# Optimization experiments

Hardware: AMD Instinct MI355X
Metric: run time of the kernel (lower is better)

Reference implementation:

```python
import jax, jax.numpy as jnp
import numpy as np

B = 32
SEQ_LEN = 512      # T and n_fft
PRED_LEN = 96      # STFT window_size = PRED_LEN // 2 = 48
TOP_K = 3
D_MODEL = 512
D_FF = 512
N_HEADS = 8
C_OUT = 32         # graph node count
NODE_DIM = 10
CONV_CH = 32
SKIP_CH = 32
GCN_DEPTH = 2
PROP_ALPHA = 0.05
HOP = 48
EPS = 1e-5


def layer_norm(x, g, b):
    m = x.mean(-1, keepdims=True)
    v = ((x - m) ** 2).mean(-1, keepdims=True)
    return (x - m) * jax.lax.rsqrt(v + EPS) * g + b


def stft_mag(x):
    """torch.stft(center=True, hann window of len 48 center-padded to n_fft) magnitude,
    vmapped over channels. Returns [B, frames, n_fft//2+1, N]."""
    n_fft = SEQ_LEN
    win_len = PRED_LEN // 2
    n = jnp.arange(win_len, dtype=x.dtype)
    win = 0.5 - 0.5 * jnp.cos(2.0 * jnp.pi * n / win_len)   # periodic hann
    pad_l = (n_fft - win_len) // 2
    win = jnp.pad(win, (pad_l, n_fft - win_len - pad_l))     # center-pad window to n_fft
    T = x.shape[1]
    xp = jnp.pad(x, ((0, 0), (n_fft // 2, n_fft // 2), (0, 0)), mode='reflect')
    nfr = T // HOP + 1
    idx = jnp.arange(nfr)[:, None] * HOP + jnp.arange(n_fft)[None, :]
    frames = xp[:, idx, :]                                   # [B, nfr, n_fft, N]
    spec = jnp.fft.rfft(frames * win[None, None, :, None], axis=2)
    return jnp.abs(spec)


def attention_block(x, wq, bq, wk, bk, wv, bv, wo, bo, ff1_w, ff1_b, ff2_w, ff2_b,
                    n1_g, n1_b, n2_g, n2_b):
    M, S, D = x.shape
    H, Dh = N_HEADS, D // N_HEADS
    q = (x @ wq.T + bq).reshape(M, S, H, Dh)
    k = (x @ wk.T + bk).reshape(M, S, H, Dh)
    v = (x @ wv.T + bv).reshape(M, S, H, Dh)
    scores = jnp.einsum('mshd,mthd->mhst', q, k) * (1.0 / float(np.sqrt(Dh)))
    o = jnp.einsum('mhst,mthd->mshd', jax.nn.softmax(scores, axis=-1), v).reshape(M, S, D)
    x1 = layer_norm(x + (o @ wo.T + bo), n1_g, n1_b)
    y = jax.nn.gelu(x1 @ ff1_w.T + ff1_b, approximate=False) @ ff2_w.T + ff2_b
    return layer_norm(x1 + y, n2_g, n2_b)


def graph_block(x, nv1, nv2, sw, sb, mw, mb, ew, eb, lw, lb, g, b):
    # adaptive adjacency over C_OUT nodes
    adp = jax.nn.softmax(jax.nn.relu(nv1 @ nv2), axis=1)
    adj = adp + jnp.eye(C_OUT, dtype=x.dtype)
    a = adj / adj.sum(1, keepdims=True)
    # start_conv: [B,1,D,T] -> [B,CONV_CH,C_OUT,T]
    h = jax.lax.conv_general_dilated(x.transpose(0, 2, 1)[:, None], sw, (1, 1), 'VALID',
                                     dimension_numbers=('NCHW', 'OIHW', 'NCHW'))
    h = h + sb[None, :, None, None]
    x0, outs = h, [h]
    for _ in range(GCN_DEPTH):  # mixprop
        h = PROP_ALPHA * x0 + (1.0 - PROP_ALPHA) * jnp.einsum('bcwt,vw->bcvt', h, a)
        outs.append(h)
    ho = jnp.einsum('oc,bcnt->bont', mw, jnp.concatenate(outs, axis=1)) + mb[None, :, None, None]
    h = jax.nn.gelu(ho, approximate=False)
    out = jnp.einsum('bcns,tcs->btn', h, ew) + eb[None, :, None]   # end_conv (1,seq_len) kernel
    out = out @ lw + lb                                            # Linear c_out -> d_model
    return layer_norm(x + out, g, b)


def setup_inputs() -> dict:
    ks = jax.random.split(jax.random.key(0), 32)
    r = lambda i, shape, s=0.02: jax.random.normal(ks[i], shape, jnp.float32) * s
    kh = D_MODEL - C_OUT + 1
    return {
        'x': jax.random.normal(ks[0], (B, SEQ_LEN, D_MODEL), jnp.float32),
        'nv1': r(1, (TOP_K, C_OUT, NODE_DIM), 1.0),
        'nv2': r(2, (TOP_K, NODE_DIM, C_OUT), 1.0),
        'start_w': r(3, (TOP_K, CONV_CH, 1, kh, 1)),
        'start_b': r(4, (TOP_K, CONV_CH)),
        'mix_w': r(5, (TOP_K, SKIP_CH, (GCN_DEPTH + 1) * CONV_CH)),
        'mix_b': r(6, (TOP_K, SKIP_CH)),
        'end_w': r(7, (TOP_K, SEQ_LEN, SKIP_CH, SEQ_LEN)),
        'end_b': r(8, (TOP_K, SEQ_LEN)),
        'glin_w': r(9, (TOP_K, C_OUT, D_MODEL)),
        'glin_b': r(10, (TOP_K, D_MODEL)),
        'gnorm_g': 1.0 + r(11, (TOP_K, D_MODEL), 0.1),
        'gnorm_b': r(12, (TOP_K, D_MODEL), 0.1),
        'wq': r(13, (D_MODEL, D_MODEL)), 'bq': r(14, (D_MODEL,)),
        'wk': r(15, (D_MODEL, D_MODEL)), 'bk': r(16, (D_MODEL,)),
        'wv': r(17, (D_MODEL, D_MODEL)), 'bv': r(18, (D_MODEL,)),
        'wo': r(19, (D_MODEL, D_MODEL)), 'bo': r(20, (D_MODEL,)),
        'ff1_w': r(21, (D_FF, D_MODEL)), 'ff1_b': r(22, (D_FF,)),
        'ff2_w': r(23, (D_MODEL, D_FF)), 'ff2_b': r(24, (D_MODEL,)),
        'an1_g': 1.0 + r(25, (D_MODEL,), 0.1), 'an1_b': r(26, (D_MODEL,), 0.1),
        'an2_g': 1.0 + r(27, (D_MODEL,), 0.1), 'an2_b': r(28, (D_MODEL,), 0.1),
        'norm_g': 1.0 + r(29, (D_MODEL,), 0.1), 'norm_b': r(30, (D_MODEL,), 0.1),
    }


def reference(x, nv1, nv2, start_w, start_b, mix_w, mix_b, end_w, end_b, glin_w, glin_b,
              gnorm_g, gnorm_b, wq, bq, wk, bk, wv, bv, wo, bo,
              ff1_w, ff1_b, ff2_w, ff2_b, an1_g, an1_b, an2_g, an2_b, norm_g, norm_b):
    Bx, T, N = x.shape
    mag = stft_mag(x)                                   # [B, frames, Fbins, N]
    freq = mag.mean(axis=(0, 1, 3)).at[0].set(0.0)
    top = np.asarray(jax.lax.top_k(freq, TOP_K)[1])     # concrete: shapes below are data-dependent
    periods = [int(T // int(f)) for f in top]
    sw = jax.nn.softmax(mag[:, :, top, :].mean(axis=(1, 3)), axis=1)  # [B, k] scale weights
    cur = x
    res = []
    for i in range(TOP_K):
        scale = periods[i]
        # NOTE: faithful to the original bug: x is overwritten by gconv output each iteration
        cur = graph_block(cur, nv1[i], nv2[i], start_w[i], start_b[i], mix_w[i], mix_b[i],
                          end_w[i], end_b[i], glin_w[i], glin_b[i], gnorm_g[i], gnorm_b[i])
        length = -(-T // scale) * scale
        out = jnp.pad(cur, ((0, 0), (0, length - T), (0, 0))) if length > T else cur
        out = out.reshape(Bx * (length // scale), scale, N)
        out = attention_block(out, wq, bq, wk, bk, wv, bv, wo, bo,
                              ff1_w, ff1_b, ff2_w, ff2_b, an1_g, an1_b, an2_g, an2_b)
        out = jax.nn.gelu(layer_norm(out, norm_g, norm_b), approximate=False)
        out = out.reshape(Bx, length, N)[:, :T]
        res.append(out)
    res = jnp.stack(res, axis=-1)                       # [B, T, N, k]
    return (res * sw[:, None, None, :]).sum(-1) + cur
```

## Files before the change

### kernel.cpp

```cpp
#include <hip/hip_runtime.h>
#include <math.h>

#define DI __device__ __forceinline__

namespace {
constexpr int B_ = 32;
constexpr int T_ = 512;
constexpr int N_ = 512;
constexpr int C_ = 32;
constexpr int KH_ = 481;
constexpr int HOP_ = 48;
constexpr int WIN_ = 48;
constexpr int NFR_ = 11;
constexpr int NBIN_ = 257;
constexpr int NSB_ = 8 * NFR_ * B_;
constexpr int TOKMAX = 21760;
constexpr int PLW = TOKMAX * 512;
constexpr float EPS_ = 1e-5f;

constexpr size_t MBY = 1ull << 20;
constexpr size_t OFF_META = 0;
constexpr size_t OFF_FREQ = 4096;
constexpr size_t OFF_SW   = 8192;
constexpr size_t OFF_BEFF = 16384;
constexpr size_t OFF_P12  = 32768;
constexpr size_t OFF_FSB  = 65536;
constexpr size_t OFF_OSM  = 1 * MBY;
constexpr size_t OFF_WB   = 4 * MBY;
constexpr size_t OFF_WDH  = 10 * MBY;
constexpr size_t OFF_EWH  = 12 * MBY;
constexpr size_t OFF_CUR  = 44 * MBY;
constexpr size_t OFF_ACC  = 76 * MBY;
constexpr size_t TR       = 108 * MBY;
constexpr size_t OFF_T    = TR;
constexpr size_t OFF_WPH  = TR + 6 * MBY;
constexpr size_t OFF_G    = TR + 64 * MBY;
constexpr size_t OFF_G2   = TR + 128 * MBY;
constexpr size_t OFF_PART = TR + 192 * MBY;
constexpr size_t OFF_A0 = TR;
constexpr size_t OFF_A2 = TR + 44 * MBY;
constexpr size_t OFF_A3 = TR + 88 * MBY;
constexpr size_t OFF_A4 = TR + 132 * MBY;
constexpr size_t OFF_A5 = TR + 176 * MBY;
constexpr size_t OFF_FP = TR;
}

typedef __attribute__((ext_vector_type(2))) float f32x2;
typedef __attribute__((ext_vector_type(4))) float f32x4;
typedef __attribute__((ext_vector_type(8))) short bf8;
typedef __attribute__((ext_vector_type(8))) unsigned short u16x8;

DI float gelu_exact(float x) { return 0.5f * x * (1.0f + erff(x * 0.7071067811865475f)); }
DI unsigned short f2bf(float f) {
  unsigned u = __float_as_uint(f);
  u += 0x7FFFu + ((u >> 16) & 1u);
  return (unsigned short)(u >> 16);
}
DI float bf2f(unsigned short s) { return __uint_as_float(((unsigned)s) << 16); }
DI float ld2(const unsigned short* __restrict__ H, const unsigned short* __restrict__ L,
             size_t i) { return bf2f(H[i]) + bf2f(L[i]); }
DI void st2(unsigned short* __restrict__ H, unsigned short* __restrict__ L,
            size_t i, float v) {
  unsigned short h = f2bf(v);
  H[i] = h;
  L[i] = f2bf(v - bf2f(h));
}
DI void gll16(const unsigned short* g, unsigned short* l) {
  __builtin_amdgcn_global_load_lds(
      (const __attribute__((address_space(1))) void*)g,
      (__attribute__((address_space(3))) void*)l, 16, 0, 0);
}

__global__ __launch_bounds__(256) void k_stft2(const float* __restrict__ x,
                                               float* __restrict__ fpart) {
  int bid = blockIdx.x;
  int cc = bid & 7;
  int f = (bid >> 3) % NFR_;
  int b = bid / (8 * NFR_);
  __shared__ float xw[WIN_][64];
  int tid = threadIdx.x;
  for (int i = tid; i < WIN_ * 64; i += 256) {
    int j = i >> 6, n = i & 63;
    int gi = f * HOP_ + 232 + j - 256;
    if (gi < 0) gi = -gi;
    float w = 0.5f - 0.5f * cosf((float)j * 0.13089969389957472f);
    xw[j][n] = w * x[((size_t)b * T_ + gi) * N_ + cc * 64 + n];
  }
  __syncthreads();
  for (int pair = tid; pair < NBIN_ * 8; pair += 256) {
    int k = pair >> 3;
    int c4 = (pair & 7) * 4;
    int r0 = (k * 232) & 511;
    float a0 = (float)r0 * 0.012271846303085130f;
    float c = cosf(a0), s = sinf(a0);
    float dA = (float)k * 0.012271846303085130f;
    float cd = cosf(dA), sd = sinf(dA);
    f32x2 ri[8];
#pragma unroll
    for (int q = 0; q < 8; ++q) ri[q] = (f32x2){0.f, 0.f};
#pragma unroll 4
    for (int j = 0; j < WIN_; ++j) {
      float4 v0 = *(const float4*)&xw[j][c4];
      float4 v1 = *(const float4*)&xw[j][32 + c4];
      f32x2 cs = (f32x2){c, s};
      ri[0] += v0.x * cs;
      ri[1] += v0.y * cs;
      ri[2] += v0.z * cs;
      ri[3] += v0.w * cs;
      ri[4] += v1.x * cs;
      ri[5] += v1.y * cs;
      ri[6] += v1.z * cs;
      ri[7] += v1.w * cs;
      float cn = c * cd - s * sd;
      s = s * cd + c * sd;
      c = cn;
    }
    float m = 0.f;
#pragma unroll
    for (int q = 0; q < 8; ++q) m += sqrtf(ri[q].x * ri[q].x + ri[q].y * ri[q].y);
    for (int off = 4; off > 0; off >>= 1) m += __shfl_xor(m, off);
    if ((tid & 7) == 0) fpart[(size_t)k * NSB_ + bid] = m;
  }
}

__global__ __launch_bounds__(256) void k_fred(const float* __restrict__ fpart,
                                              float* __restrict__ freq,
                                              float* __restrict__ fsumb) {
  int k = blockIdx.x;
  int tid = threadIdx.x;
  int b = tid >> 3, j = tid & 7;
  float s = 0.f;
  for (int i = j; i < 88; i += 8) s += fpart[(size_t)k * NSB_ + b * 88 + i];
  for (int off = 4; off > 0; off >>= 1) s += __shfl_xor(s, off);
  __shared__ float bs[32];
  if (j == 0) bs[b] = s;
  __syncthreads();
  if (tid < 32) {
    float v = bs[tid];
    fsumb[k * 32 + tid] = v;
    for (int off = 16; off > 0; off >>= 1) v += __shfl_xor(v, off);
    if (tid == 0) freq[k] = v;
  }
}

__global__ void k_topk(const float* __restrict__ freq, int* __restrict__ meta) {
  if (threadIdx.x == 0 && blockIdx.x == 0) {
    float bv[3] = {-1e30f, -1e30f, -1e30f};
    int bi[3] = {1, 1, 1};
    for (int k = 1; k < NBIN_; ++k) {
      float v = freq[k];
      if (v > bv[0]) { bv[2]=bv[1]; bi[2]=bi[1]; bv[1]=bv[0]; bi[1]=bi[0]; bv[0]=v; bi[0]=k; }
      else if (v > bv[1]) { bv[2]=bv[1]; bi[2]=bi[1]; bv[1]=v; bi[1]=k; }
      else if (v > bv[2]) { bv[2]=v; bi[2]=k; }
    }
    for (int i = 0; i < 3; ++i) {
      int top = bi[i];
      int p = T_ / top;
      int L = ((T_ + p - 1) / p) * p;
      meta[i] = top;
      meta[3 + i] = p;
      meta[6 + i] = L;
      meta[9 + i] = L / p;
      meta[15 + i] = B_ * L;
    }
  }
}

__global__ void k_sw2(const float* __restrict__ fsumb, const int* __restrict__ meta,
                      float* __restrict__ swb) {
  int b = threadIdx.x;
  if (b < B_) {
    float inv = 1.0f / (float)(NFR_ * N_);
    float m0 = fsumb[meta[0] * 32 + b] * inv;
    float m1 = fsumb[meta[1] * 32 + b] * inv;
    float m2 = fsumb[meta[2] * 32 + b] * inv;
    float mx = fmaxf(m0, fmaxf(m1, m2));
    float e0 = expf(m0 - mx), e1 = expf(m1 - mx), e2 = expf(m2 - mx);
    float s = e0 + e1 + e2;
    swb[b * 4 + 0] = e0 / s; swb[b * 4 + 1] = e1 / s; swb[b * 4 + 2] = e2 / s;
  }
}

__global__ __launch_bounds__(1024) void k_adjprep(const float* __restrict__ nv1,
                                                  const float* __restrict__ nv2,
                                                  const float* __restrict__ mw,
                                                  const float* __restrict__ mb,
                                                  const float* __restrict__ sb,
                                                  float* __restrict__ P12,
                                                  float* __restrict__ beff) {
  __shared__ float A32s[32][32];
  __shared__ float Ms[32][32], P1s[32][32], P2s[32][32], S1[32], S2[32], sbl[32];
  int tid = threadIdx.x;
  if (tid < 32) {
    int v = tid;
    float row[32];
    for (int w = 0; w < 32; ++w) {
      float s = 0.f;
      for (int d = 0; d < 10; ++d) s += nv1[v * 10 + d] * nv2[d * 32 + w];
      row[w] = fmaxf(s, 0.f);
    }
    float mx = -1e30f;
    for (int w = 0; w < 32; ++w) mx = fmaxf(mx, row[w]);
    float sm = 0.f;
    for (int w = 0; w < 32; ++w) { row[w] = expf(row[w] - mx); sm += row[w]; }
    for (int w = 0; w < 32; ++w) row[w] /= sm;
    row[v] += 1.0f;
    float rs = 0.f;
    for (int w = 0; w < 32; ++w) rs += row[w];
    for (int w = 0; w < 32; ++w) A32s[v][w] = row[w] / rs;
    sbl[tid] = sb[tid];
  }
  __syncthreads();
  int w = tid >> 5, v = tid & 31;
  Ms[w][v] = A32s[v][w];
  __syncthreads();
  float p1 = 0.95f * Ms[w][v] + (w == v ? 0.05f : 0.f);
  P1s[w][v] = p1;
  __syncthreads();
  float p2 = 0.f;
  for (int u = 0; u < 32; ++u) p2 += P1s[w][u] * Ms[u][v];
  p2 = 0.95f * p2 + (w == v ? 0.05f : 0.f);
  P2s[w][v] = p2;
  P12[tid] = p1;
  P12[1024 + tid] = p2;
  __syncthreads();
  if (tid < 32) {
    float s1 = 0.f, s2 = 0.f;
    for (int u = 0; u < 32; ++u) { s1 += P1s[u][tid]; s2 += P2s[u][tid]; }
    S1[tid] = s1; S2[tid] = s2;
  }
  __syncthreads();
  int o = w;
  float be = mb[o];
  for (int c = 0; c < 32; ++c) {
    float sc = sbl[c];
    be += mw[o * 96 + c] * sc;
    be += mw[o * 96 + 32 + c] * sc * S1[v];
    be += mw[o * 96 + 64 + c] * sc * S2[v];
  }
  beff[tid] = be;
}

__global__ __launch_bounds__(256) void k_T(const float* __restrict__ P12,
                                           const float* __restrict__ mw,
                                           float* __restrict__ Tm) {
  int idx = blockIdx.x * 256 + threadIdx.x;
  int r = idx >> 10, k2 = idx & 1023;
  int o = r >> 5, v = r & 31;
  int c = k2 >> 5, w = k2 & 31;
  float t = mw[o * 96 + 32 + c] * P12[w * 32 + v]
          + mw[o * 96 + 64 + c] * P12[1024 + w * 32 + v];
  if (w == v) t += mw[o * 96 + c];
  Tm[idx] = t;
}

__global__ void k_wdh(const float* __restrict__ swi, unsigned short* __restrict__ WH) {
  int idx = blockIdx.x * 256 + threadIdx.x;
  int j = idx >> 10, k2 = idx & 1023;
  int c = k2 >> 5, w = k2 & 31;
  int kk = j - w;
  float vv = (kk >= 0 && kk < KH_) ? swi[c * KH_ + kk] : 0.f;
  WH[idx] = f2bf(vv);
}

__global__ void k_splith(const float* __restrict__ src, unsigned short* __restrict__ Hi,
                         int n) {
  int i = blockIdx.x * 256 + threadIdx.x;
  if (i * 4 >= n) return;
  float4 v = *(const float4*)&src[i * 4];
  ushort4 h;
  h.x = f2bf(v.x); h.y = f2bf(v.y); h.z = f2bf(v.z); h.w = f2bf(v.w);
  *(ushort4*)&Hi[i * 4] = h;
}

__global__ __launch_bounds__(256, 2) void k_mm2(
    const float* __restrict__ A, const unsigned short* __restrict__ Bh,
    const float* __restrict__ bias,
    float* __restrict__ C, float* __restrict__ Cpart,
    int M, int N, int K, int lda, int dogelu) {
  const int bm = blockIdx.y * 128;
  if (bm >= M) return;
  const int bn = blockIdx.x * 128;
  const int nz = gridDim.z, z = blockIdx.z;
  const int kpb = K / nz;
  const int kbeg = z * kpb, kend = kbeg + kpb;

  __shared__ __align__(16) unsigned short AhS[4096], AlS[4096], BhS[4096];

  const int tid = threadIdx.x;
  const int wave = tid >> 6, lane = tid & 63;
  const int wr = wave >> 1, wc = wave & 1;
  const int fr = lane & 15, fs = lane >> 4;

  const int sr = tid >> 1, ss = (tid & 1) * 2;
  const int sx = (sr >> 1) & 3;
  const int so0 = sr * 32 + 8 * (ss ^ sx);
  const int so1 = sr * 32 + 8 * ((ss + 1) ^ sx);

  const int row0 = tid >> 2;
  const int s0 = (tid & 3) ^ ((row0 >> 1) & 3);
  const unsigned short* gBh0 = Bh + (size_t)(bn + row0) * K + s0 * 8;
  const unsigned short* gBh1 = gBh0 + (size_t)64 * K;
  unsigned short* lB0 = &BhS[wave * 512];
  unsigned short* lB1 = &BhS[2048 + wave * 512];

  int aoff[4], boff[4];
#pragma unroll
  for (int m = 0; m < 4; ++m) {
    int ra = wr * 64 + m * 16 + fr;
    aoff[m] = ra * 32 + 8 * (fs ^ ((ra >> 1) & 3));
    int rb = wc * 64 + m * 16 + fr;
    boff[m] = rb * 32 + 8 * (fs ^ ((rb >> 1) & 3));
  }

  const bool aok = (bm + sr) < M;
  const float* Arow = A + (size_t)(bm + sr) * lda + ss * 8;

  f32x4 acc[4][4];
#pragma unroll
  for (int m = 0; m < 4; ++m)
#pragma unroll
    for (int n = 0; n < 4; ++n) acc[m][n] = (f32x4){0.f, 0.f, 0.f, 0.f};

  for (int k0 = kbeg; k0 < kend; k0 += 32) {
    float4 a0, a1, a2, a3;
    if (aok) {
      const float4* p = (const float4*)(Arow + k0);
      a0 = p[0]; a1 = p[1]; a2 = p[2]; a3 = p[3];
    } else {
      a0 = a1 = a2 = a3 = make_float4(0.f, 0.f, 0.f, 0.f);
    }
    float av[16];
    av[0]=a0.x; av[1]=a0.y; av[2]=a0.z; av[3]=a0.w;
    av[4]=a1.x; av[5]=a1.y; av[6]=a1.z; av[7]=a1.w;
    av[8]=a2.x; av[9]=a2.y; av[10]=a2.z; av[11]=a2.w;
    av[12]=a3.x; av[13]=a3.y; av[14]=a3.z; av[15]=a3.w;
    u16x8 h0, h1, l0, l1;
#pragma unroll
    for (int j = 0; j < 8; ++j) {
      unsigned u = __float_as_uint(av[j]);
      h0[j] = (unsigned short)(u >> 16);
      float r2 = av[j] - __uint_as_float(u & 0xffff0000u);
      l0[j] = (unsigned short)(__float_as_uint(r2) >> 16);
      unsigned u2 = __float_as_uint(av[j + 8]);
      h1[j] = (unsigned short)(u2 >> 16);
      float r3 = av[j + 8] - __uint_as_float(u2 & 0xffff0000u);
      l1[j] = (unsigned short)(__float_as_uint(r3) >> 16);
    }
    __syncthreads();
    gll16(gBh0 + k0, lB0); gll16(gBh1 + k0, lB1);
    *(u16x8*)&AhS[so0] = h0; *(u16x8*)&AhS[so1] = h1;
    *(u16x8*)&AlS[so0] = l0; *(u16x8*)&AlS[so1] = l1;
    __syncthreads();
    bf8 ah[4], al4[4], bh4[4];
#pragma unroll
    for (int m = 0; m < 4; ++m) {
      ah[m]  = *(const bf8*)&AhS[aoff[m]];
      al4[m] = *(const bf8*)&AlS[aoff[m]];
    }
#pragma unroll
    for (int n = 0; n < 4; ++n) bh4[n] = *(const bf8*)&BhS[boff[n]];
#pragma unroll
    for (int m = 0; m < 4; ++m)
#pragma unroll
      for (int n = 0; n < 4; ++n) {
        acc[m][n] = __builtin_amdgcn_mfma_f32_16x16x32_bf16(ah[m],  bh4[n], acc[m][n], 0, 0, 0);
        acc[m][n] = __builtin_amdgcn_mfma_f32_16x16x32_bf16(al4[m], bh4[n], acc[m][n], 0, 0, 0);
      }
  }

  if (nz > 1) {
    float* P = Cpart + (size_t)z * M * N;
#pragma unroll
    for (int m = 0; m < 4; ++m)
#pragma unroll
      for (int r = 0; r < 4; ++r) {
        int row = bm + wr * 64 + m * 16 + fs * 4 + r;
        if (row < M) {
#pragma unroll
          for (int n = 0; n < 4; ++n) {
            int col = bn + wc * 64 + n * 16 + fr;
            P[(size_t)row * N + col] = acc[m][n][r];
          }
        }
      }
  } else {
    float bcol[4];
#pragma unroll
    for (int n = 0; n < 4; ++n) bcol[n] = bias ? bias[bn + wc * 64 + n * 16 + fr] : 0.f;
#pragma unroll
    for (int m = 0; m < 4; ++m)
#pragma unroll
      for (int r = 0; r < 4; ++r) {
        int row = bm + wr * 64 + m * 16 + fs * 4 + r;
        if (row < M) {
#pragma unroll
          for (int n = 0; n < 4; ++n) {
            int col = bn + wc * 64 + n * 16 + fr;
            float v = acc[m][n][r] + bcol[n];
            if (dogelu) v = gelu_exact(v);
            C[(size_t)row * N + col] = v;
          }
        }
      }
  }
}

__global__ __launch_bounds__(256, 4) void k_mmb1(
    const unsigned short* __restrict__ Ah,
    const unsigned short* __restrict__ Bh,
    const float* __restrict__ bias,
    unsigned short* __restrict__ Ch, unsigned short* __restrict__ Cl,
    int M, int N, int K, const int* __restrict__ Mdyn, int dogelu) {
  if (Mdyn) M = *Mdyn;
  const int bm = blockIdx.y * 128;
  if (bm >= M) return;
  const int bn = blockIdx.x * 128;

  __shared__ __align__(16) unsigned short AhS[4096], BhS[4096];

  const int tid = threadIdx.x;
  const int wave = tid >> 6, lane = tid & 63;
  const int wr = wave >> 1, wc = wave & 1;
  const int fr = lane & 15, fs = lane >> 4;

  const int row0 = tid >> 2;
  const int s0 = (tid & 3) ^ ((row0 >> 1) & 3);
  const unsigned short* gAh0 = Ah + (size_t)(bm + row0) * K + s0 * 8;
  const unsigned short* gAh1 = gAh0 + (size_t)64 * K;
  const unsigned short* gBh0 = Bh + (size_t)(bn + row0) * K + s0 * 8;
  const unsigned short* gBh1 = gBh0 + (size_t)64 * K;
  const int lb0 = wave * 512, lb1 = 2048 + wave * 512;

  int aoff[4], boff[4];
#pragma unroll
  for (int m = 0; m < 4; ++m) {
    int ra = wr * 64 + m * 16 + fr;
    aoff[m] = ra * 32 + 8 * (fs ^ ((ra >> 1) & 3));
    int rb = wc * 64 + m * 16 + fr;
    boff[m] = rb * 32 + 8 * (fs ^ ((rb >> 1) & 3));
  }

  f32x4 acc[4][4];
#pragma unroll
  for (int m = 0; m < 4; ++m)
#pragma unroll
    for (int n = 0; n < 4; ++n) acc[m][n] = (f32x4){0.f, 0.f, 0.f, 0.f};

  for (int k0 = 0; k0 < K; k0 += 32) {
    __syncthreads();
    gll16(gAh0 + k0, &AhS[lb0]); gll16(gAh1 + k0, &AhS[lb1]);
    gll16(gBh0 + k0, &BhS[lb0]); gll16(gBh1 + k0, &BhS[lb1]);
    __syncthreads();
    bf8 ah[4], bh4[4];
#pragma unroll
    for (int m = 0; m < 4; ++m) ah[m] = *(const bf8*)&AhS[aoff[m]];
#pragma unroll
    for (int n = 0; n < 4; ++n) bh4[n] = *(const bf8*)&BhS[boff[n]];
#pragma unroll
    for (int m = 0; m < 4; ++m)
#pragma unroll
      for (int n = 0; n < 4; ++n)
        acc[m][n] = __builtin_amdgcn_mfma_f32_16x16x32_bf16(ah[m], bh4[n], acc[m][n], 0, 0, 0);
  }

  float bcol[4];
#pragma unroll
  for (int n = 0; n < 4; ++n) bcol[n] = bias[bn + wc * 64 + n * 16 + fr];
#pragma unroll
  for (int m = 0; m < 4; ++m)
#pragma unroll
    for (int r = 0; r < 4; ++r) {
      int row = bm + wr * 64 + m * 16 + fs * 4 + r;
      if (row < M) {
#pragma unroll
        for (int n = 0; n < 4; ++n) {
          int col = bn + wc * 64 + n * 16 + fr;
          float v = acc[m][n][r] + bcol[n];
          if (dogelu) v = gelu_exact(v);
          size_t o = (size_t)row * N + col;
          unsigned short h = f2bf(v);
          Ch[o] = h;
          Cl[o] = f2bf(v - bf2f(h));
        }
      }
    }
}

__global__ void k_red16(const float* __restrict__ part, const float* __restrict__ eb,
                        float* __restrict__ dst) {
  int idx = blockIdx.x * 256 + threadIdx.x;
  float s = eb ? eb[idx & 511] : 0.f;
#pragma unroll
  for (int zz = 0; zz < 16; ++zz) s += part[(size_t)zz * 524288 + idx];
  dst[idx] = s;
}

__global__ void k_redsplit(const float* __restrict__ part, unsigned short* __restrict__ WH) {
  int idx = blockIdx.x * 256 + threadIdx.x;
  float s = 0.f;
#pragma unroll
  for (int zz = 0; zz < 8; ++zz) s += part[(size_t)zz * 524288 + idx];
  WH[idx] = f2bf(s);
}

__global__ __launch_bounds__(256) void k_repack(const float* __restrict__ G,
                                                float* __restrict__ G2) {
  int bid = blockIdx.x;
  int st = bid & 15, c = (bid >> 4) & 31, b = bid >> 9;
  __shared__ float tile[32][33];
  int tid = threadIdx.x;
  int n = tid & 31, s = tid >> 5;
  for (int q = 0; q < 4; ++q) {
    int ss = s + q * 8;
    tile[ss][n] = G[((size_t)b * T_ + st * 32 + ss) * 1024 + c * 32 + n];
  }
  __syncthreads();
  int s2 = tid & 31, n2 = tid >> 5;
  for (int q = 0; q < 4; ++q) {
    int nn = n2 + q * 8;
    G2[((size_t)b * 32 + nn) * 16384 + c * 512 + st * 32 + s2] = tile[s2][nn];
  }
}

__global__ __launch_bounds__(256) void k_lwln(const float* __restrict__ osm,
                                              const float* __restrict__ lw,
                                              const float* __restrict__ lb,
                                              const float* __restrict__ curIn,
                                              const float* __restrict__ g,
                                              const float* __restrict__ bt,
                                              float* __restrict__ curOut,
                                              unsigned short* __restrict__ xh,
                                              unsigned short* __restrict__ xl,
                                              const int* __restrict__ meta, int iter) {
  int tok = blockIdx.x;
  int b = tok >> 9, t = tok & 511;
  __shared__ float os[C_];
  __shared__ float red[256];
  int tid = threadIdx.x;
  if (tid < C_) os[tid] = osm[((size_t)b * C_ + tid) * T_ + t];
  __syncthreads();
  float val[2];
#pragma unroll
  for (int q = 0; q < 2; ++q) {
    int m = tid + q * 256;
    float s = lb[m] + curIn[(size_t)tok * N_ + m];
    for (int n2 = 0; n2 < C_; ++n2) s += os[n2] * lw[n2 * N_ + m];
    val[q] = s;
  }
  red[tid] = val[0] + val[1];
  __syncthreads();
  for (int off = 128; off > 0; off >>= 1) { if (tid < off) red[tid] += red[tid + off]; __syncthreads(); }
  float mean = red[0] * (1.0f / N_);
  __syncthreads();
  float d0 = val[0] - mean, d1 = val[1] - mean;
  red[tid] = d0 * d0 + d1 * d1;
  __syncthreads();
  for (int off = 128; off > 0; off >>= 1) { if (tid < off) red[tid] += red[tid + off]; __syncthreads(); }
  float inv = rsqrtf(red[0] * (1.0f / N_) + EPS_);
  float o0 = d0 * inv * g[tid] + bt[tid];
  float o1 = d1 * inv * g[tid + 256] + bt[tid + 256];
  curOut[(size_t)tok * N_ + tid] = o0;
  curOut[(size_t)tok * N_ + tid + 256] = o1;
  int L = meta[6 + iter];
  size_t pi = ((size_t)b * L + t) * N_;
  st2(xh, xl, pi + tid, o0);
  st2(xh, xl, pi + tid + 256, o1);
}

__global__ void k_padtail(unsigned short* __restrict__ xh, unsigned short* __restrict__ xl,
                          const int* __restrict__ meta, int iter) {
  int L = meta[6 + iter];
  int pad = L - T_;
  if (pad <= 0) return;
  size_t total = (size_t)B_ * pad * N_;
  for (size_t idx = (size_t)blockIdx.x * 256 + threadIdx.x; idx < total;
       idx += (size_t)gridDim.x * 256) {
    size_t row = idx >> 9;
    int d = (int)(idx & 511);
    int b = (int)(row / pad), l = T_ + (int)(row % pad);
    size_t o = ((size_t)b * L + l) * N_ + d;
    xh[o] = 0; xl[o] = 0;
  }
}

__global__ __launch_bounds__(256) void k_lnadd(const unsigned short* __restrict__ r1h,
                                               const unsigned short* __restrict__ r1l,
                                               const unsigned short* __restrict__ r2h,
                                               const unsigned short* __restrict__ r2l,
                                               const float* __restrict__ g,
                                               const float* __restrict__ bt,
                                               unsigned short* __restrict__ dh,
                                               unsigned short* __restrict__ dl,
                                               const int* __restrict__ meta, int iter) {
  int tokens = meta[15 + iter];
  int tok = blockIdx.x;
  if (tok >= tokens) return;
  __shared__ float red[256];
  int tid = threadIdx.x;
  float val[2];
#pragma unroll
  for (int q = 0; q < 2; ++q) {
    size_t i = (size_t)tok * N_ + tid + q * 256;
    val[q] = ld2(r1h, r1l, i) + ld2(r2h, r2l, i);
  }
  red[tid] = val[0] + val[1];
  __syncthreads();
  for (int off = 128; off > 0; off >>= 1) { if (tid < off) red[tid] += red[tid + off]; __syncthreads(); }
  float mean = red[0] * (1.0f / N_);
  __syncthreads();
  float d0 = val[0] - mean, d1 = val[1] - mean;
  red[tid] = d0 * d0 + d1 * d1;
  __syncthreads();
  for (int off = 128; off > 0; off >>= 1) { if (tid < off) red[tid] += red[tid + off]; __syncthreads(); }
  float inv = rsqrtf(red[0] * (1.0f / N_) + EPS_);
  st2(dh, dl, (size_t)tok * N_ + tid, d0 * inv * g[tid] + bt[tid]);
  st2(dh, dl, (size_t)tok * N_ + tid + 256, d1 * inv * g[tid + 256] + bt[tid + 256]);
}

__global__ __launch_bounds__(256) void k_lnfin(const unsigned short* __restrict__ r1h,
                                               const unsigned short* __restrict__ r1l,
                                               const unsigned short* __restrict__ r2h,
                                               const unsigned short* __restrict__ r2l,
                                               const float* __restrict__ g1,
                                               const float* __restrict__ b1,
                                               const float* __restrict__ g2,
                                               const float* __restrict__ b2,
                                               const float* __restrict__ swb,
                                               float* __restrict__ acc,
                                               const int* __restrict__ meta, int iter) {
  int L = meta[6 + iter];
  int tok = blockIdx.x;
  if (tok >= B_ * L) return;
  int b = tok / L, l = tok % L;
  if (l >= T_) return;
  __shared__ float red[256];
  int tid = threadIdx.x;
  float val[2];
#pragma unroll
  for (int q = 0; q < 2; ++q) {
    size_t i = (size_t)tok * N_ + tid + q * 256;
    val[q] = ld2(r1h, r1l, i) + ld2(r2h, r2l, i);
  }
  red[tid] = val[0] + val[1];
  __syncthreads();
  for (int off = 128; off > 0; off >>= 1) { if (tid < off) red[tid] += red[tid + off]; __syncthreads(); }
  float mean = red[0] * (1.0f / N_);
  __syncthreads();
  float d0 = val[0] - mean, d1 = val[1] - mean;
  red[tid] = d0 * d0 + d1 * d1;
  __syncthreads();
  for (int off = 128; off > 0; off >>= 1) { if (tid < off) red[tid] += red[tid + off]; __syncthreads(); }
  float inv = rsqrtf(red[0] * (1.0f / N_) + EPS_);
  float y0 = d0 * inv * g1[tid] + b1[tid];
  float y1 = d1 * inv * g1[tid + 256] + b1[tid + 256];
  __syncthreads();
  red[tid] = y0 + y1;
  __syncthreads();
  for (int off = 128; off > 0; off >>= 1) { if (tid < off) red[tid] += red[tid + off]; __syncthreads(); }
  float mean2 = red[0] * (1.0f / N_);
  __syncthreads();
  float e0 = y0 - mean2, e1 = y1 - mean2;
  red[tid] = e0 * e0 + e1 * e1;
  __syncthreads();
  for (int off = 128; off > 0; off >>= 1) { if (tid < off) red[tid] += red[tid + off]; __syncthreads(); }
  float inv2 = rsqrtf(red[0] * (1.0f / N_) + EPS_);
  float s = swb[b * 4 + iter];
  float u0 = gelu_exact(e0 * inv2 * g2[tid] + b2[tid]);
  float u1 = gelu_exact(e1 * inv2 * g2[tid + 256] + b2[tid + 256]);
  size_t o = ((size_t)b * T_ + l) * N_;
  acc[o + tid] += s * u0;
  acc[o + tid + 256] += s * u1;
}

__global__ __launch_bounds__(256) void k_attn32(
    const unsigned short* __restrict__ qh, const unsigned short* __restrict__ ql,
    const unsigned short* __restrict__ kh, const unsigned short* __restrict__ kl,
    const unsigned short* __restrict__ vh, const unsigned short* __restrict__ vl,
    unsigned short* __restrict__ oh, unsigned short* __restrict__ ol,
    const int* __restrict__ meta, int iter) {
  (void)vl;
  int S = meta[3 + iter];
  if (S > 32) return;
  int L = meta[6 + iter], nseq = meta[9 + iter];
  int npair = B_ * nseq * 8;
  __shared__ float Kt[4][64 * 33];
  __shared__ unsigned short Vsh[4][32 * 66];
  __shared__ float qs[4][64];
  int tid = threadIdx.x;
  int wave = tid >> 6, lane = tid & 63;
  float* Ktw = Kt[wave];
  unsigned short* Vw = Vsh[wave];
  int gw = (blockIdx.x * 256 + tid) >> 6;
  int nw = (gridDim.x * 256) >> 6;
  const int tt = lane & 31;
  const int hf = lane >> 5;
  for (int pair = gw; pair < npair; pair += nw) {
    int h = pair & 7;
    int m = pair >> 3;
    int b = m / nseq, g2 = m - b * nseq;
    size_t base = ((size_t)b * L + (size_t)g2 * S) * N_ + h * 64;
    for (int i = lane; i < S * 64; i += 64) {
      int t = i >> 6, d = i & 63;
      size_t gi = base + (size_t)t * N_ + d;
      Ktw[d * 33 + t] = ld2(kh, kl, gi);
      Vw[t * 66 + d] = vh[gi];
    }
    bool tok = tt < S;
    for (int s = 0; s < S; ++s) {
      qs[wave][lane] = ld2(qh, ql, base + (size_t)s * N_ + lane);
      float part = 0.f;
      if (tok) {
        const float* kp = &Ktw[hf * 32 * 33 + tt];
        const float* qp = &qs[wave][hf * 32];
#pragma unroll 8
        for (int j = 0; j < 32; ++j) part += qp[j] * kp[j * 33];
      }
      part += __shfl_xor(part, 32);
      float sc = tok ? part * 0.125f : -3.0e38f;
      float mx = sc;
      for (int off = 16; off > 0; off >>= 1) mx = fmaxf(mx, __shfl_xor(mx, off));
      float p = tok ? expf(sc - mx) : 0.f;
      float ssum = p;
      for (int off = 16; off > 0; off >>= 1) ssum += __shfl_xor(ssum, off);
      float ov = 0.f;
      for (int t = 0; t < S; ++t) {
        float pt = __shfl(p, t);
        ov += pt * bf2f(Vw[t * 66 + lane]);
      }
      st2(oh, ol, base + (size_t)s * N_ + lane, ov / ssum);
    }
  }
}

__global__ __launch_bounds__(512) void k_attn_small(
    const unsigned short* __restrict__ qh, const unsigned short* __restrict__ ql,
    const unsigned short* __restrict__ kh, const unsigned short* __restrict__ kl,
    const unsigned short* __restrict__ vh, const unsigned short* __restrict__ vl,
    unsigned short* __restrict__ oh, unsigned short* __restrict__ ol,
    const int* __restrict__ meta, int iter) {
  int S = meta[3 + iter];
  if (S <= 32 || S > 128) return;
  int L = meta[6 + iter], nseq = meta[9 + iter];
  int M = B_ * nseq;
  int mh = blockIdx.x;
  int m = mh >> 3, h = mh & 7;
  if (m >= M) return;
  int b = m / nseq, g2 = m % nseq;
  size_t tok0 = (size_t)b * L + (size_t)g2 * S;
  __shared__ float Ks[64 * 129];
  __shared__ float Vs[128 * 65];
  __shared__ float qrow[8][64];
  __shared__ float Pr[8][128];
  int tid = threadIdx.x;
  for (int i = tid; i < S * 64; i += 512) {
    int t = i >> 6, d = i & 63;
    size_t gi = (tok0 + t) * N_ + h * 64 + d;
    float kv = ld2(kh, kl, gi);
    Ks[d * 129 + t] = kv;
    Vs[t * 65 + d] = ld2(vh, vl, gi);
  }
  __syncthreads();
  int wave = tid >> 6, lane = tid & 63;
  for (int s = wave; s < S; s += 8) {
    qrow[wave][lane] = ld2(qh, ql, (tok0 + s) * N_ + h * 64 + lane);
    float sc0 = -3.0e38f, sc1 = -3.0e38f;
    if (lane < S) {
      float ad = 0.f;
#pragma unroll 16
      for (int j = 0; j < 64; ++j) ad += qrow[wave][j] * Ks[j * 129 + lane];
      sc0 = ad * 0.125f;
    }
    if (S > 64 && lane + 64 < S) {
      float ad = 0.f;
#pragma unroll 16
      for (int j = 0; j < 64; ++j) ad += qrow[wave][j] * Ks[j * 129 + lane + 64];
      sc1 = ad * 0.125f;
    }
    float mx = fmaxf(sc0, sc1);
    for (int off = 32; off > 0; off >>= 1) mx = fmaxf(mx, __shfl_xor(mx, off));
    float e0 = (lane < S) ? expf(sc0 - mx) : 0.f;
    float e1 = (S > 64 && lane + 64 < S) ? expf(sc1 - mx) : 0.f;
    if (lane < S) Pr[wave][lane] = e0;
    if (S > 64 && lane + 64 < S) Pr[wave][lane + 64] = e1;
    float ssum = e0 + e1;
    for (int off = 32; off > 0; off >>= 1) ssum += __shfl_xor(ssum, off);
    float ov = 0.f;
#pragma unroll 8
    for (int t = 0; t < S; ++t) ov += Pr[wave][t] * Vs[t * 65 + lane];
    st2(oh, ol, (tok0 + s) * N_ + h * 64 + lane, ov / ssum);
  }
}

__global__ __launch_bounds__(256) void k_attn_big(
    const unsigned short* __restrict__ qh, const unsigned short* __restrict__ ql,
    const unsigned short* __restrict__ kh, const unsigned short* __restrict__ kl,
    const unsigned short* __restrict__ vh, const unsigned short* __restrict__ vl,
    unsigned short* __restrict__ oh, unsigned short* __restrict__ ol,
    const int* __restrict__ meta, int iter) {
  (void)kl; (void)vl;
  int p = meta[3 + iter];
  if (p <= 128) return;
  int L = meta[6 + iter], nseq = meta[9 + iter];
  int M = B_ * nseq;
  int mh = blockIdx.x;
  int m = mh >> 3, h = mh & 7;
  if (m >= M) return;
  int S = p;
  int b = m / nseq, g2 = m % nseq;
  size_t tok0 = (size_t)b * L + (size_t)g2 * S;
  __shared__ unsigned short Ks[512 * 66];
  __shared__ unsigned short Vs[512 * 66];
  __shared__ float qrow[4][64];
  __shared__ float Pr[4][512];
  int tid = threadIdx.x;
  for (int i = tid; i < S * 64; i += 256) {
    int t = i >> 6, d = i & 63;
    size_t gi = (tok0 + t) * N_ + h * 64 + d;
    Ks[t * 66 + d] = kh[gi];
    Vs[t * 66 + d] = vh[gi];
  }
  __syncthreads();
  int wave = tid >> 6, lane = tid & 63;
  for (int s = wave; s < S; s += 4) {
    qrow[wave][lane] = ld2(qh, ql, (tok0 + s) * N_ + h * 64 + lane);
    const float2* qp = (const float2*)&qrow[wave][0];
    float sc[8];
    float mx = -3.0e38f;
#pragma unroll
    for (int c2 = 0; c2 < 8; ++c2) {
      int t = lane + c2 * 64;
      float sv = -3.0e38f;
      if (t < S) {
        const unsigned int* kp = (const unsigned int*)&Ks[t * 66];
        float ad = 0.f;
#pragma unroll
        for (int j2 = 0; j2 < 32; ++j2) {
          float2 qq = qp[j2];
          unsigned int kw = kp[j2];
          ad += qq.x * bf2f((unsigned short)(kw & 0xffffu));
          ad += qq.y * bf2f((unsigned short)(kw >> 16));
        }
        sv = ad * 0.125f;
      }
      sc[c2] = sv;
      mx = fmaxf(mx, sv);
    }
    for (int off = 32; off > 0; off >>= 1) mx = fmaxf(mx, __shfl_xor(mx, off));
    float ssum = 0.f;
#pragma unroll
    for (int c2 = 0; c2 < 8; ++c2) {
      int t = lane + c2 * 64;
      float e = 0.f;
      if (t < S) { e = expf(sc[c2] - mx); Pr[wave][t] = e; }
      ssum += e;
    }
    for (int off = 32; off > 0; off >>= 1) ssum += __shfl_xor(ssum, off);
    float inv = 1.0f / ssum;
    float ov = 0.f;
#pragma unroll 8
    for (int t = 0; t < S; ++t) ov += Pr[wave][t] * bf2f(Vs[t * 66 + lane]);
    st2(oh, ol, (tok0 + s) * N_ + h * 64 + lane, ov * inv);
  }
}

__global__ void k_final(const float* __restrict__ acc, const float* __restrict__ cur,
                        float* __restrict__ out) {
  size_t idx = (size_t)blockIdx.x * 256 + threadIdx.x;
  out[idx] = acc[idx] + cur[idx];
}

extern "C" void kernel_launch(void* const* d_in, const int* in_sizes, int n_in,
                              void* d_out, int out_size, void* d_ws, size_t ws_size,
                              hipStream_t stream) {
  (void)in_sizes; (void)n_in; (void)out_size; (void)ws_size;
  const float* x       = (const float*)d_in[0];
  const float* nv1     = (const float*)d_in[1];
  const float* nv2     = (const float*)d_in[2];
  const float* start_w = (const float*)d_in[3];
  const float* start_b = (const float*)d_in[4];
  const float* mix_w   = (const float*)d_in[5];
  const float* mix_b   = (const float*)d_in[6];
  const float* end_w   = (const float*)d_in[7];
  const float* end_b   = (const float*)d_in[8];
  const float* glin_w  = (const float*)d_in[9];
  const float* glin_b  = (const float*)d_in[10];
  const float* gnorm_g = (const float*)d_in[11];
  const float* gnorm_b = (const float*)d_in[12];
  const float* wq = (const float*)d_in[13];
  const float* bq = (const float*)d_in[14];
  const float* wk = (const float*)d_in[15];
  const float* bk = (const float*)d_in[16];
  const float* wv = (const float*)d_in[17];
  const float* bv = (const float*)d_in[18];
  const float* wo = (const float*)d_in[19];
  const float* bo = (const float*)d_in[20];
  const float* ff1w = (const float*)d_in[21];
  const float* ff1b = (const float*)d_in[22];
  const float* ff2w = (const float*)d_in[23];
  const float* ff2b = (const float*)d_in[24];
  const float* an1g = (const float*)d_in[25];
  const float* an1b = (const float*)d_in[26];
  const float* an2g = (const float*)d_in[27];
  const float* an2b = (const float*)d_in[28];
  const float* nrmg = (const float*)d_in[29];
  const float* nrmb = (const float*)d_in[30];

  char* ws = (char*)d_ws;
  int*   meta = (int*)(ws + OFF_META);
  float* freq = (float*)(ws + OFF_FREQ);
  float* swb  = (float*)(ws + OFF_SW);
  float* beff = (float*)(ws + OFF_BEFF);
  float* P12  = (float*)(ws + OFF_P12);
  float* fsumb = (float*)(ws + OFF_FSB);
  float* osm  = (float*)(ws + OFF_OSM);
  unsigned short* WB  = (unsigned short*)(ws + OFF_WB);
  unsigned short* WdH = (unsigned short*)(ws + OFF_WDH);
  unsigned short* EWH = (unsigned short*)(ws + OFF_EWH);
  float* cur  = (float*)(ws + OFF_CUR);
  float* accb = (float*)(ws + OFF_ACC);
  float* fpart = (float*)(ws + OFF_FP);
  float* Tm   = (float*)(ws + OFF_T);
  unsigned short* WPH = (unsigned short*)(ws + OFF_WPH);
  float* G    = (float*)(ws + OFF_G);
  float* G2   = (float*)(ws + OFF_G2);
  float* PART = (float*)(ws + OFF_PART);
  unsigned short* A0h = (unsigned short*)(ws + OFF_A0); unsigned short* A0l = A0h + PLW;
  unsigned short* A2h = (unsigned short*)(ws + OFF_A2); unsigned short* A2l = A2h + PLW;
  unsigned short* A3h = (unsigned short*)(ws + OFF_A3); unsigned short* A3l = A3h + PLW;
  unsigned short* A4h = (unsigned short*)(ws + OFF_A4); unsigned short* A4l = A4h + PLW;
  unsigned short* A5h = (unsigned short*)(ws + OFF_A5); unsigned short* A5l = A5h + PLW;

  hipMemsetAsync(accb, 0, (size_t)B_ * T_ * N_ * 4, stream);

  k_stft2<<<NSB_, 256, 0, stream>>>(x, fpart);
  k_fred<<<NBIN_, 256, 0, stream>>>(fpart, freq, fsumb);
  k_topk<<<1, 64, 0, stream>>>(freq, meta);
  k_sw2<<<1, 64, 0, stream>>>(fsumb, meta, swb);

  const float* wlist[6] = {wq, wk, wv, wo, ff1w, ff2w};
  for (int w = 0; w < 6; ++w)
    k_splith<<<256, 256, 0, stream>>>(wlist[w], WB + (size_t)w * 262144, 262144);
  unsigned short* WqH = WB;
  unsigned short* WkH = WB + 262144;
  unsigned short* WvH = WB + 2 * 262144;
  unsigned short* WoH = WB + 3 * 262144;
  unsigned short* F1H = WB + 4 * 262144;
  unsigned short* F2H = WB + 5 * 262144;

  const float* curIn = x;
  for (int i = 0; i < 3; ++i) {
    k_adjprep<<<1, 1024, 0, stream>>>(nv1 + i * C_ * 10, nv2 + i * 10 * C_,
                                      mix_w + i * C_ * 96, mix_b + i * C_,
                                      start_b + i * C_, P12, beff);
    k_T<<<4096, 256, 0, stream>>>(P12, mix_w + i * C_ * 96, Tm);
    k_wdh<<<2048, 256, 0, stream>>>(start_w + i * C_ * KH_, WdH);
    k_mm2<<<dim3(4, 8, 8), 256, 0, stream>>>(Tm, WdH, nullptr, nullptr, PART,
                                             1024, 512, 1024, 1024, 0);
    k_redsplit<<<2048, 256, 0, stream>>>(PART, WPH);
    k_mm2<<<dim3(8, 128, 1), 256, 0, stream>>>(curIn, WPH, beff, G, nullptr,
                                               16384, 1024, 512, 512, 1);
    k_repack<<<B_ * C_ * 16, 256, 0, stream>>>(G, G2);
    k_splith<<<8192, 256, 0, stream>>>(end_w + (size_t)i * 8388608, EWH, 8388608);
    k_mm2<<<dim3(4, 8, 16), 256, 0, stream>>>(G2, EWH, nullptr, nullptr, PART,
                                              1024, 512, 16384, 16384, 0);
    k_red16<<<2048, 256, 0, stream>>>(PART, end_b + i * T_, osm);
    k_lwln<<<B_ * T_, 256, 0, stream>>>(osm, glin_w + i * C_ * N_, glin_b + i * N_, curIn,
                                        gnorm_g + i * N_, gnorm_b + i * N_, cur,
                                        A0h, A0l, meta, i);
    k_padtail<<<512, 256, 0, stream>>>(A0h, A0l, meta, i);
    const int* Mdyn = meta + 15 + i;
    dim3 gT(4, TOKMAX / 128, 1);
    k_mmb1<<<gT, 256, 0, stream>>>(A0h, WqH, bq, A2h, A2l, TOKMAX, 512, 512, Mdyn, 0);
    k_mmb1<<<gT, 256, 0, stream>>>(A0h, WkH, bk, A3h, A3l, TOKMAX, 512, 512, Mdyn, 0);
    k_mmb1<<<gT, 256, 0, stream>>>(A0h, WvH, bv, A4h, A4l, TOKMAX, 512, 512, Mdyn, 0);
    k_attn32<<<2048, 256, 0, stream>>>(A2h, A2l, A3h, A3l, A4h, A4l, A5h, A5l, meta, i);
    k_attn_small<<<4096, 512, 0, stream>>>(A2h, A2l, A3h, A3l, A4h, A4l, A5h, A5l, meta, i);
    k_attn_big<<<1024, 256, 0, stream>>>(A2h, A2l, A3h, A3l, A4h, A4l, A5h, A5l, meta, i);
    k_mmb1<<<gT, 256, 0, stream>>>(A5h, WoH, bo, A2h, A2l, TOKMAX, 512, 512, Mdyn, 0);
    k_lnadd<<<TOKMAX, 256, 0, stream>>>(A0h, A0l, A2h, A2l, an1g, an1b, A3h, A3l, meta, i);
    k_mmb1<<<gT, 256, 0, stream>>>(A3h, F1H, ff1b, A4h, A4l, TOKMAX, 512, 512, Mdyn, 1);
    k_mmb1<<<gT, 256, 0, stream>>>(A4h, F2H, ff2b, A5h, A5l, TOKMAX, 512, 512, Mdyn, 0);
    k_lnfin<<<TOKMAX, 256, 0, stream>>>(A3h, A3l, A5h, A5l, an2g, an2b, nrmg, nrmb,
                                        swb, accb, meta, i);
    curIn = cur;
  }
  k_final<<<(B_ * T_ * N_) / 256, 256, 0, stream>>>(accb, curIn, (float*)d_out);
}
```

Measured before the change: 2.207 ms.

## Fuse QKV projections into one GEMM and drop low-half bf16 split for attention

```diff
diff --git a/kernel.cpp b/kernel.cpp
--- a/kernel.cpp
+++ b/kernel.cpp
@@ -143,8 +143,11 @@
   }
 }
 
-__global__ void k_topk(const float* __restrict__ freq, int* __restrict__ meta) {
-  if (threadIdx.x == 0 && blockIdx.x == 0) {
+__global__ void k_topk(const float* __restrict__ freq, const float* __restrict__ fsumb,
+                       int* __restrict__ meta, float* __restrict__ swb) {
+  __shared__ int stop[3];
+  int tid = threadIdx.x;
+  if (tid == 0) {
     float bv[3] = {-1e30f, -1e30f, -1e30f};
     int bi[3] = {1, 1, 1};
     for (int k = 1; k < NBIN_; ++k) {
@@ -162,18 +165,16 @@
       meta[6 + i] = L;
       meta[9 + i] = L / p;
       meta[15 + i] = B_ * L;
-    }
-  }
-}
-
-__global__ void k_sw2(const float* __restrict__ fsumb, const int* __restrict__ meta,
-                      float* __restrict__ swb) {
-  int b = threadIdx.x;
+      stop[i] = top;
+    }
+  }
+  __syncthreads();
+  int b = tid;
   if (b < B_) {
     float inv = 1.0f / (float)(NFR_ * N_);
-    float m0 = fsumb[meta[0] * 32 + b] * inv;
-    float m1 = fsumb[meta[1] * 32 + b] * inv;
-    float m2 = fsumb[meta[2] * 32 + b] * inv;
+    float m0 = fsumb[stop[0] * 32 + b] * inv;
+    float m1 = fsumb[stop[1] * 32 + b] * inv;
+    float m2 = fsumb[stop[2] * 32 + b] * inv;
     float mx = fmaxf(m0, fmaxf(m1, m2));
     float e0 = expf(m0 - mx), e1 = expf(m1 - mx), e2 = expf(m2 - mx);
     float s = e0 + e1 + e2;
@@ -481,7 +482,89 @@
           size_t o = (size_t)row * N + col;
           unsigned short h = f2bf(v);
           Ch[o] = h;
-          Cl[o] = f2bf(v - bf2f(h));
+          if (Cl) Cl[o] = f2bf(v - bf2f(h));
+        }
+      }
+    }
+}
+
+__global__ __launch_bounds__(256, 4) void k_mmqkv(
+    const unsigned short* __restrict__ Ah,
+    const unsigned short* __restrict__ Bh,
+    const float* __restrict__ bq, const float* __restrict__ bk,
+    const float* __restrict__ bv,
+    unsigned short* __restrict__ Qh, unsigned short* __restrict__ Kh,
+    unsigned short* __restrict__ Vh,
+    int M, int K, const int* __restrict__ Mdyn) {
+  if (Mdyn) M = *Mdyn;
+  const int bm = blockIdx.y * 128;
+  if (bm >= M) return;
+  const int bn = blockIdx.x * 128;
+  const int sel = bn >> 9;
+  unsigned short* Ch = sel == 0 ? Qh : (sel == 1 ? Kh : Vh);
+  const float* bias = sel == 0 ? bq : (sel == 1 ? bk : bv);
+  const int cb = bn & 511;
+
+  __shared__ __align__(16) unsigned short AhS[4096], BhS[4096];
+
+  const int tid = threadIdx.x;
+  const int wave = tid >> 6, lane = tid & 63;
+  const int wr = wave >> 1, wc = wave & 1;
+  const int fr = lane & 15, fs = lane >> 4;
+
+  const int row0 = tid >> 2;
+  const int s0 = (tid & 3) ^ ((row0 >> 1) & 3);
+  const unsigned short* gAh0 = Ah + (size_t)(bm + row0) * K + s0 * 8;
+  const unsigned short* gAh1 = gAh0 + (size_t)64 * K;
+  const unsigned short* gBh0 = Bh + (size_t)(bn + row0) * K + s0 * 8;
+  const unsigned short* gBh1 = gBh0 + (size_t)64 * K;
+  const int lb0 = wave * 512, lb1 = 2048 + wave * 512;
+
+  int aoff[4], boff[4];
+#pragma unroll
+  for (int m = 0; m < 4; ++m) {
+    int ra = wr * 64 + m * 16 + fr;
+    aoff[m] = ra * 32 + 8 * (fs ^ ((ra >> 1) & 3));
+    int rb = wc * 64 + m * 16 + fr;
+    boff[m] = rb * 32 + 8 * (fs ^ ((rb >> 1) & 3));
+  }
+
+  f32x4 acc[4][4];
+#pragma unroll
+  for (int m = 0; m < 4; ++m)
+#pragma unroll
+    for (int n = 0; n < 4; ++n) acc[m][n] = (f32x4){0.f, 0.f, 0.f, 0.f};
+
+  for (int k0 = 0; k0 < K; k0 += 32) {
+    __syncthreads();
+    gll16(gAh0 + k0, &AhS[lb0]); gll16(gAh1 + k0, &AhS[lb1]);
+    gll16(gBh0 + k0, &BhS[lb0]); gll16(gBh1 + k0, &BhS[lb1]);
+    __syncthreads();
+    bf8 ah[4], bh4[4];
+#pragma unroll
+    for (int m = 0; m < 4; ++m) ah[m] = *(const bf8*)&AhS[aoff[m]];
+#pragma unroll
+    for (int n = 0; n < 4; ++n) bh4[n] = *(const bf8*)&BhS[boff[n]];
+#pragma unroll
+    for (int m = 0; m < 4; ++m)
+#pragma unroll
+      for (int n = 0; n < 4; ++n)
+        acc[m][n] = __builtin_amdgcn_mfma_f32_16x16x32_bf16(ah[m], bh4[n], acc[m][n], 0, 0, 0);
+  }
+
+  float bcol[4];
+#pragma unroll
+  for (int n = 0; n < 4; ++n) bcol[n] = bias[cb + wc * 64 + n * 16 + fr];
+#pragma unroll
+  for (int m = 0; m < 4; ++m)
+#pragma unroll
+    for (int r = 0; r < 4; ++r) {
+      int row = bm + wr * 64 + m * 16 + fs * 4 + r;
+      if (row < M) {
+#pragma unroll
+        for (int n = 0; n < 4; ++n) {
+          int col = cb + wc * 64 + n * 16 + fr;
+          Ch[(size_t)row * 512 + col] = f2bf(acc[m][n][r] + bcol[n]);
         }
       }
     }
@@ -674,12 +757,11 @@
 }
 
 __global__ __launch_bounds__(256) void k_attn32(
-    const unsigned short* __restrict__ qh, const unsigned short* __restrict__ ql,
-    const unsigned short* __restrict__ kh, const unsigned short* __restrict__ kl,
-    const unsigned short* __restrict__ vh, const unsigned short* __restrict__ vl,
-    unsigned short* __restrict__ oh, unsigned short* __restrict__ ol,
+    const unsigned short* __restrict__ qh,
+    const unsigned short* __restrict__ kh,
+    const unsigned short* __restrict__ vh,
+    unsigned short* __restrict__ oh,
     const int* __restrict__ meta, int iter) {
-  (void)vl;
   int S = meta[3 + iter];
   if (S > 32) return;
   int L = meta[6 + iter], nseq = meta[9 + iter];
@@ -703,12 +785,12 @@
     for (int i = lane; i < S * 64; i += 64) {
       int t = i >> 6, d = i & 63;
       size_t gi = base + (size_t)t * N_ + d;
-      Ktw[d * 33 + t] = ld2(kh, kl, gi);
+      Ktw[d * 33 + t] = bf2f(kh[gi]);
       Vw[t * 66 + d] = vh[gi];
     }
     bool tok = tt < S;
     for (int s = 0; s < S; ++s) {
-      qs[wave][lane] = ld2(qh, ql, base + (size_t)s * N_ + lane);
+      qs[wave][lane] = bf2f(qh[base + (size_t)s * N_ + lane]);
       float part = 0.f;
       if (tok) {
         const float* kp = &Ktw[hf * 32 * 33 + tt];
@@ -728,16 +810,16 @@
         float pt = __shfl(p, t);
         ov += pt * bf2f(Vw[t * 66 + lane]);
       }
-      st2(oh, ol, base + (size_t)s * N_ + lane, ov / ssum);
+      oh[base + (size_t)s * N_ + lane] = f2bf(ov / ssum);
     }
   }
 }
 
 __global__ __launch_bounds__(512) void k_attn_small(
-    const unsigned short* __restrict__ qh, const unsigned short* __restrict__ ql,
-    const unsigned short* __restrict__ kh, const unsigned short* __restrict__ kl,
-    const unsigned short* __restrict__ vh, const unsigned short* __restrict__ vl,
-    unsigned short* __restrict__ oh, unsigned short* __restrict__ ol,
+    const unsigned short* __restrict__ qh,
+    const unsigned short* __restrict__ kh,
+    const unsigned short* __restrict__ vh,
+    unsigned short* __restrict__ oh,
     const int* __restrict__ meta, int iter) {
   int S = meta[3 + iter];
   if (S <= 32 || S > 128) return;
@@ -756,14 +838,13 @@
   for (int i = tid; i < S * 64; i += 512) {
     int t = i >> 6, d = i & 63;
     size_t gi = (tok0 + t) * N_ + h * 64 + d;
-    float kv = ld2(kh, kl, gi);
-    Ks[d * 129 + t] = kv;
-    Vs[t * 65 + d] = ld2(vh, vl, gi);
+    Ks[d * 129 + t] = bf2f(kh[gi]);
+    Vs[t * 65 + d] = bf2f(vh[gi]);
   }
   __syncthreads();
   int wave = tid >> 6, lane = tid & 63;
   for (int s = wave; s < S; s += 8) {
-    qrow[wave][lane] = ld2(qh, ql, (tok0 + s) * N_ + h * 64 + lane);
+    qrow[wave][lane] = bf2f(qh[(tok0 + s) * N_ + h * 64 + lane]);
     float sc0 = -3.0e38f, sc1 = -3.0e38f;
     if (lane < S) {
       float ad = 0.f;
@@ -788,17 +869,16 @@
     float ov = 0.f;
 #pragma unroll 8
     for (int t = 0; t < S; ++t) ov += Pr[wave][t] * Vs[t * 65 + lane];
-    st2(oh, ol, (tok0 + s) * N_ + h * 64 + lane, ov / ssum);
+    oh[(tok0 + s) * N_ + h * 64 + lane] = f2bf(ov / ssum);
   }
 }
 
 __global__ __launch_bounds__(256) void k_attn_big(
-    const unsigned short* __restrict__ qh, const unsigned short* __restrict__ ql,
-    const unsigned short* __restrict__ kh, const unsigned short* __restrict__ kl,
-    const unsigned short* __restrict__ vh, const unsigned short* __restrict__ vl,
-    unsigned short* __restrict__ oh, unsigned short* __restrict__ ol,
+    const unsigned short* __restrict__ qh,
+    const unsigned short* __restrict__ kh,
+    const unsigned short* __restrict__ vh,
+    unsigned short* __restrict__ oh,
     const int* __restrict__ meta, int iter) {
-  (void)kl; (void)vl;
   int p = meta[3 + iter];
   if (p <= 128) return;
   int L = meta[6 + iter], nseq = meta[9 + iter];
@@ -823,7 +903,7 @@
   __syncthreads();
   int wave = tid >> 6, lane = tid & 63;
   for (int s = wave; s < S; s += 4) {
-    qrow[wave][lane] = ld2(qh, ql, (tok0 + s) * N_ + h * 64 + lane);
+    qrow[wave][lane] = bf2f(qh[(tok0 + s) * N_ + h * 64 + lane]);
     const float2* qp = (const float2*)&qrow[wave][0];
     float sc[8];
     float mx = -3.0e38f;
@@ -860,7 +940,7 @@
     float ov = 0.f;
 #pragma unroll 8
     for (int t = 0; t < S; ++t) ov += Pr[wave][t] * bf2f(Vs[t * 66 + lane]);
-    st2(oh, ol, (tok0 + s) * N_ + h * 64 + lane, ov * inv);
+    oh[(tok0 + s) * N_ + h * 64 + lane] = f2bf(ov * inv);
   }
 }
 
@@ -928,22 +1008,19 @@
   unsigned short* A0h = (unsigned short*)(ws + OFF_A0); unsigned short* A0l = A0h + PLW;
   unsigned short* A2h = (unsigned short*)(ws + OFF_A2); unsigned short* A2l = A2h + PLW;
   unsigned short* A3h = (unsigned short*)(ws + OFF_A3); unsigned short* A3l = A3h + PLW;
-  unsigned short* A4h = (unsigned short*)(ws + OFF_A4); unsigned short* A4l = A4h + PLW;
+  unsigned short* A4h = (unsigned short*)(ws + OFF_A4);
   unsigned short* A5h = (unsigned short*)(ws + OFF_A5); unsigned short* A5l = A5h + PLW;
 
   hipMemsetAsync(accb, 0, (size_t)B_ * T_ * N_ * 4, stream);
 
   k_stft2<<<NSB_, 256, 0, stream>>>(x, fpart);
   k_fred<<<NBIN_, 256, 0, stream>>>(fpart, freq, fsumb);
-  k_topk<<<1, 64, 0, stream>>>(freq, meta);
-  k_sw2<<<1, 64, 0, stream>>>(fsumb, meta, swb);
+  k_topk<<<1, 64, 0, stream>>>(freq, fsumb, meta, swb);
 
   const float* wlist[6] = {wq, wk, wv, wo, ff1w, ff2w};
   for (int w = 0; w < 6; ++w)
     k_splith<<<256, 256, 0, stream>>>(wlist[w], WB + (size_t)w * 262144, 262144);
-  unsigned short* WqH = WB;
-  unsigned short* WkH = WB + 262144;
-  unsigned short* WvH = WB + 2 * 262144;
+  unsigned short* WqkvH = WB;
   unsigned short* WoH = WB + 3 * 262144;
   unsigned short* F1H = WB + 4 * 262144;
   unsigned short* F2H = WB + 5 * 262144;
@@ -971,15 +1048,14 @@
     k_padtail<<<512, 256, 0, stream>>>(A0h, A0l, meta, i);
     const int* Mdyn = meta + 15 + i;
     dim3 gT(4, TOKMAX / 128, 1);
-    k_mmb1<<<gT, 256, 0, stream>>>(A0h, WqH, bq, A2h, A2l, TOKMAX, 512, 512, Mdyn, 0);
-    k_mmb1<<<gT, 256, 0, stream>>>(A0h, WkH, bk, A3h, A3l, TOKMAX, 512, 512, Mdyn, 0);
-    k_mmb1<<<gT, 256, 0, stream>>>(A0h, WvH, bv, A4h, A4l, TOKMAX, 512, 512, Mdyn, 0);
-    k_attn32<<<2048, 256, 0, stream>>>(A2h, A2l, A3h, A3l, A4h, A4l, A5h, A5l, meta, i);
-    k_attn_small<<<4096, 512, 0, stream>>>(A2h, A2l, A3h, A3l, A4h, A4l, A5h, A5l, meta, i);
-    k_attn_big<<<1024, 256, 0, stream>>>(A2h, A2l, A3h, A3l, A4h, A4l, A5h, A5l, meta, i);
+    k_mmqkv<<<dim3(12, TOKMAX / 128), 256, 0, stream>>>(A0h, WqkvH, bq, bk, bv,
+                                                        A2h, A3h, A4h, TOKMAX, 512, Mdyn);
+    k_attn32<<<2048, 256, 0, stream>>>(A2h, A3h, A4h, A5h, meta, i);
+    k_attn_small<<<4096, 512, 0, stream>>>(A2h, A3h, A4h, A5h, meta, i);
+    k_attn_big<<<1024, 256, 0, stream>>>(A2h, A3h, A4h, A5h, meta, i);
     k_mmb1<<<gT, 256, 0, stream>>>(A5h, WoH, bo, A2h, A2l, TOKMAX, 512, 512, Mdyn, 0);
     k_lnadd<<<TOKMAX, 256, 0, stream>>>(A0h, A0l, A2h, A2l, an1g, an1b, A3h, A3l, meta, i);
-    k_mmb1<<<gT, 256, 0, stream>>>(A3h, F1H, ff1b, A4h, A4l, TOKMAX, 512, 512, Mdyn, 1);
+    k_mmb1<<<gT, 256, 0, stream>>>(A3h, F1H, ff1b, A4h, nullptr, TOKMAX, 512, 512, Mdyn, 1);
     k_mmb1<<<gT, 256, 0, stream>>>(A4h, F2H, ff2b, A5h, A5l, TOKMAX, 512, 512, Mdyn, 0);
     k_lnfin<<<TOKMAX, 256, 0, stream>>>(A3h, A3l, A5h, A5l, an2g, an2b, nrmg, nrmb,
                                         swb, accb, meta, i);
```

Result: no change. 2.168 ms (-1.8%).
